# Kernel optimization log

Hardware: AMD Instinct MI355X
Metric: run time of the kernel (lower is better)

## Reference

```python
import jax, jax.numpy as jnp
import numpy as np

N = 4096
E = 262144
IN_C = 128
OUT_C = 128
EDGE_D = 16


def setup_inputs() -> dict:
    key = jax.random.key(0)
    k = jax.random.split(key, 8)
    x = jax.random.normal(k[0], (N, IN_C), dtype=jnp.float32)
    edge_index = jax.random.randint(k[1], (2, E), 0, N, dtype=jnp.int64)
    edge_attr = jax.random.normal(k[2], (N, N, EDGE_D), dtype=jnp.float32)
    # nn.Linear params: y = x @ W.T + b; store pre-transposed W for x @ W
    s1 = 1.0 / np.sqrt(IN_C + EDGE_D)
    s2 = 1.0 / np.sqrt(OUT_C)
    W1 = jax.random.uniform(k[3], (IN_C + EDGE_D, OUT_C), jnp.float32, -s1, s1)
    b1 = jax.random.uniform(k[4], (OUT_C,), jnp.float32, -s1, s1)
    W2 = jax.random.uniform(k[5], (OUT_C, OUT_C), jnp.float32, -s2, s2)
    b2 = jax.random.uniform(k[6], (OUT_C,), jnp.float32, -s2, s2)
    return {"x": x, "edge_index": edge_index, "edge_attr": edge_attr,
            "W1": W1, "b1": b1, "W2": W2, "b2": b2}


def reference(x, edge_index, edge_attr, W1, b1, W2, b2):
    row, col = edge_index[0], edge_index[1]
    x_row = x[row]                      # [E, IN_C] gather
    e = edge_attr[row, col]             # [E, EDGE_D] gather from dense NxN table
    h = jnp.concatenate([x_row, e], axis=-1)     # [E, IN_C+EDGE_D]
    h = jax.nn.relu(h @ W1 + b1)                  # [E, OUT_C]
    h = jax.nn.relu(h @ W2 + b2)                  # [E, OUT_C]
    # global_add_pool(out, col): scatter-add edges into node buckets by col
    return jax.ops.segment_sum(h, col, num_segments=x.shape[0])  # [N, OUT_C]
```

## Files before the change

kernel.cpp:

```cpp
#include <hip/hip_runtime.h>
#include <hip/hip_bf16.h>

#define NN 4096
#define IC 128
#define OC 128
#define ED 16
#define EPB 128
#define NT 512
#define NSLOT 8
#define NBLK 256

typedef __bf16 bf16x8 __attribute__((ext_vector_type(8)));
typedef float  f32x4  __attribute__((ext_vector_type(4)));

#define BAR() do { asm volatile("s_waitcnt lgkmcnt(0)" ::: "memory"); \
    __builtin_amdgcn_s_barrier(); \
    __builtin_amdgcn_sched_barrier(0); } while (0)

__device__ __forceinline__ unsigned short bf16u(float f) {
    unsigned int u = __float_as_uint(f);
    u = (u + 0x7FFFu + ((u >> 16) & 1u)) >> 16;
    return (unsigned short)u;
}
__device__ __forceinline__ float bf16tof(unsigned short h) {
    return __uint_as_float(((unsigned int)h) << 16);
}
__device__ __forceinline__ int swzk(int row) { return (row ^ (row >> 3)) & 7; }

__global__ __launch_bounds__(128) void k_xw1(
    const float* __restrict__ x, const float* __restrict__ W1,
    const float* __restrict__ b1, float* __restrict__ xw1b,
    float* __restrict__ out, int* __restrict__ hist)
{
    __shared__ float xs[8][IC];
    const int t = threadIdx.x;
    const int r0 = blockIdx.x * 8;
    #pragma unroll
    for (int r = 0; r < 8; ++r) xs[r][t] = x[(size_t)(r0 + r) * IC + t];

    const float4 z = make_float4(0.f, 0.f, 0.f, 0.f);
    float4* o4 = (float4*)out;
    o4[blockIdx.x * 256 + t]       = z;
    o4[blockIdx.x * 256 + 128 + t] = z;
    if (blockIdx.x == 0) {
        int4* h4 = (int4*)hist;
        #pragma unroll
        for (int j = 0; j < 8; ++j) h4[j * 128 + t] = make_int4(0, 0, 0, 0);
    }

    __syncthreads();
    float acc[8];
    const float bb = b1[t];
    #pragma unroll
    for (int r = 0; r < 8; ++r) acc[r] = bb;
    #pragma unroll 4
    for (int k = 0; k < IC; ++k) {
        const float w = W1[(size_t)k * OC + t];
        #pragma unroll
        for (int r = 0; r < 8; ++r) acc[r] = fmaf(xs[r][k], w, acc[r]);
    }
    #pragma unroll
    for (int r = 0; r < 8; ++r) xw1b[(size_t)(r0 + r) * OC + t] = acc[r];
}

__global__ void k_hist(const int* __restrict__ eidx, int* __restrict__ hist, int E) {
    const int i = blockIdx.x * blockDim.x + threadIdx.x;
    if (i < E) atomicAdd(&hist[eidx[E + i]], 1);
}

__global__ __launch_bounds__(256) void k_scan(
    const int* __restrict__ hist, int* __restrict__ cursor)
{
    __shared__ int tot[256];
    __shared__ int base[256];
    const int t = threadIdx.x;
    int loc[16];
    int s = 0;
    #pragma unroll
    for (int j = 0; j < 16; ++j) { loc[j] = s; s += hist[t * 16 + j]; }
    tot[t] = s;
    __syncthreads();
    if (t == 0) {
        int a = 0;
        for (int i = 0; i < 256; ++i) { base[i] = a; a += tot[i]; }
    }
    __syncthreads();
    const int b = base[t];
    #pragma unroll
    for (int j = 0; j < 16; ++j) cursor[t * 16 + j] = b + loc[j];
}

__global__ void k_scatter(const int* __restrict__ eidx, int* __restrict__ cursor,
                          int2* __restrict__ csr, int E) {
    const int i = blockIdx.x * blockDim.x + threadIdx.x;
    if (i < E) {
        const int row = eidx[i];
        const int col = eidx[E + i];
        const int pos = atomicAdd(&cursor[col], 1);
        csr[pos] = make_int2(row, col);
    }
}

__global__ __launch_bounds__(NT, 2) void k_edge6(
    const int2* __restrict__ csr, const float* __restrict__ eattr,
    const float* __restrict__ xw1b, const float* __restrict__ W1,
    const float* __restrict__ W2, const float* __restrict__ b2,
    float* __restrict__ out, int E)
{
    extern __shared__ char smem[];
    char*   const W2hi = smem;
    char*   const W2lo = smem + 32768;
    char*   const h1hi = smem + 65536;
    char*   const h1lo = smem + 98304;
    float4* const eaL  = (float4*)(smem + 131072);
    float4* const w1L  = (float4*)(smem + 139264);
    float*  const lacc = (float*)(smem + 147456);
    int*    const srowL = (int*)(smem + 151552);
    int*    const scolL = srowL + 256;

    const int t   = threadIdx.x;
    const int l   = t & 63;
    const int wid = t >> 6;
    const int cg  = t & 15, eg = t >> 4;
    const int c0  = cg << 3, e0 = eg << 2;
    const int sz  = (eg >> 1) & 3;
    const int em  = t >> 2, q = t & 3;
    const int esz = (em >> 3) & 3;

    w1L[t] = ((const float4*)(W1 + (size_t)IC * OC))[t];
    {
        const int n = t >> 2, kh = (t & 3) * 32;
        const int key = swzk(n) << 4;
        for (int j0 = 0; j0 < 32; j0 += 8) {
            union { unsigned short us[8]; uint4 qv; } Hh, Hl;
            #pragma unroll
            for (int j = 0; j < 8; ++j) {
                const float w = W2[(size_t)(kh + j0 + j) * OC + n];
                const unsigned short h = bf16u(w);
                Hh.us[j] = h;
                Hl.us[j] = bf16u(w - bf16tof(h));
            }
            const int a = n * 256 + (((kh + j0) * 2) ^ key);
            *(uint4*)(W2hi + a) = Hh.qv;
            *(uint4*)(W2lo + a) = Hl.qv;
        }
    }
    float b2r[8];
    #pragma unroll
    for (int nr = 0; nr < 8; ++nr) b2r[nr] = b2[nr * 16 + (l & 15)];

    const int nper = (E / EPB) / NBLK;
    const int ibb  = blockIdx.x * nper;

    if (t < EPB) {
        const int2 rc = csr[(size_t)ibb * EPB + t];
        srowL[t] = rc.x;
        scolL[t] = rc.y;
    }
    __syncthreads();

    float4 pA;
    {
        const int r = srowL[em], c = scolL[em];
        pA = ((const float4*)(eattr + ((size_t)r * NN + c) * ED))[q];
    }
    float4 xa[4], xb[4];
    #pragma unroll
    for (int ri = 0; ri < 4; ++ri) {
        const int row = srowL[e0 + ri];
        const float4* p = (const float4*)(xw1b + (size_t)row * OC + c0);
        xa[ri] = p[0]; xb[ri] = p[1];
    }
    int2 pidx;
    {
        const int ibn = (nper > 1) ? 1 : 0;
        pidx = (t < EPB) ? csr[(size_t)(ibb + ibn) * EPB + t] : make_int2(0, 0);
    }

    int cur = 0;
    for (int ii = 0; ii < nper; ++ii) {
        const int nxt = cur ^ 1;

        BAR();

        lacc[t] = 0.f; lacc[t + NT] = 0.f;
        if (t < EPB) { srowL[nxt * 128 + t] = pidx.x; scolL[nxt * 128 + t] = pidx.y; }
        eaL[(em * 4 + q) ^ esz] = pA;
        BAR();

        float4 ha[4], hb[4];
        #pragma unroll
        for (int ri = 0; ri < 4; ++ri) { ha[ri] = xa[ri]; hb[ri] = xb[ri]; }
        #pragma unroll
        for (int dc = 0; dc < 4; ++dc) {
            float4 ev[4];
            #pragma unroll
            for (int ri = 0; ri < 4; ++ri)
                ev[ri] = eaL[((e0 + ri) * 4 + dc) ^ sz];
            #pragma unroll
            for (int dd = 0; dd < 4; ++dd) {
                const int d = dc * 4 + dd;
                const float4 wA = w1L[d * 32 + cg * 2];
                const float4 wB = w1L[d * 32 + cg * 2 + 1];
                #pragma unroll
                for (int ri = 0; ri < 4; ++ri) {
                    const float evd = (dd == 0) ? ev[ri].x : (dd == 1) ? ev[ri].y
                                     : (dd == 2) ? ev[ri].z : ev[ri].w;
                    ha[ri].x = fmaf(evd, wA.x, ha[ri].x);
                    ha[ri].y = fmaf(evd, wA.y, ha[ri].y);
                    ha[ri].z = fmaf(evd, wA.z, ha[ri].z);
                    ha[ri].w = fmaf(evd, wA.w, ha[ri].w);
                    hb[ri].x = fmaf(evd, wB.x, hb[ri].x);
                    hb[ri].y = fmaf(evd, wB.y, hb[ri].y);
                    hb[ri].z = fmaf(evd, wB.z, hb[ri].z);
                    hb[ri].w = fmaf(evd, wB.w, hb[ri].w);
                }
            }
        }
        #pragma unroll
        for (int ri = 0; ri < 4; ++ri) {
            const int row = e0 + ri;
            float v[8] = { ha[ri].x, ha[ri].y, ha[ri].z, ha[ri].w,
                           hb[ri].x, hb[ri].y, hb[ri].z, hb[ri].w };
            union { unsigned short us[8]; uint4 qv; } Hh, Hl;
            #pragma unroll
            for (int j = 0; j < 8; ++j) {
                const float f = fmaxf(v[j], 0.f);
                const unsigned short h = bf16u(f);
                Hh.us[j] = h;
                Hl.us[j] = bf16u(f - bf16tof(h));
            }
            const int boff = (cg * 16) ^ (swzk(row) << 4);
            *(uint4*)(h1hi + row * 256 + boff) = Hh.qv;
            *(uint4*)(h1lo + row * 256 + boff) = Hl.qv;
        }

        {
            const int r = srowL[nxt * 128 + em], c = scolL[nxt * 128 + em];
            pA = ((const float4*)(eattr + ((size_t)r * NN + c) * ED))[q];
        }
        #pragma unroll
        for (int ri = 0; ri < 4; ++ri) {
            const int row = srowL[nxt * 128 + e0 + ri];
            const float4* p = (const float4*)(xw1b + (size_t)row * OC + c0);
            xa[ri] = p[0]; xb[ri] = p[1];
        }
        {
            const int iin = (ii + 2 < nper) ? (ii + 2) : (nper - 1);
            pidx = (t < EPB) ? csr[(size_t)(ibb + iin) * EPB + t] : make_int2(0, 0);
        }
        BAR();

        f32x4 acc[8];
        #pragma unroll
        for (int nr = 0; nr < 8; ++nr) acc[nr] = (f32x4){0.f, 0.f, 0.f, 0.f};
        const int arow = wid * 16 + (l & 15);
        const int akey = swzk(arow) << 4;
        #pragma unroll
        for (int kc = 0; kc < 4; ++kc) {
            const int kb = kc * 64 + ((l >> 4) << 4);
            const bf16x8 aH = *(const bf16x8*)(h1hi + arow * 256 + (kb ^ akey));
            const bf16x8 aL = *(const bf16x8*)(h1lo + arow * 256 + (kb ^ akey));
            #pragma unroll
            for (int nr = 0; nr < 8; ++nr) {
                const int brow = nr * 16 + (l & 15);
                const int ba = brow * 256 + (kb ^ (swzk(brow) << 4));
                const bf16x8 bH = *(const bf16x8*)(W2hi + ba);
                const bf16x8 bL = *(const bf16x8*)(W2lo + ba);
                acc[nr] = __builtin_amdgcn_mfma_f32_16x16x32_bf16(aH, bH, acc[nr], 0, 0, 0);
                acc[nr] = __builtin_amdgcn_mfma_f32_16x16x32_bf16(aL, bH, acc[nr], 0, 0, 0);
                acc[nr] = __builtin_amdgcn_mfma_f32_16x16x32_bf16(aH, bL, acc[nr], 0, 0, 0);
            }
        }

        const int colbase = scolL[cur * 128];
        {
            const int eb = wid * 16 + ((l >> 4) << 2);
            float s[8];
            int ccur = scolL[cur * 128 + eb];
            #pragma unroll
            for (int nr = 0; nr < 8; ++nr)
                s[nr] = fmaxf(acc[nr][0] + b2r[nr], 0.f);
            #pragma unroll
            for (int r = 1; r < 4; ++r) {
                const int c = scolL[cur * 128 + eb + r];
                if (c != ccur) {
                    const int slot = ccur - colbase;
                    if (slot < NSLOT) {
                        #pragma unroll
                        for (int nr = 0; nr < 8; ++nr)
                            if (s[nr] != 0.f)
                                atomicAdd(&lacc[slot * OC + nr * 16 + (l & 15)], s[nr]);
                    } else {
                        #pragma unroll
                        for (int nr = 0; nr < 8; ++nr)
                            if (s[nr] != 0.f)
                                atomicAdd(&out[(size_t)ccur * OC + nr * 16 + (l & 15)], s[nr]);
                    }
                    ccur = c;
                    #pragma unroll
                    for (int nr = 0; nr < 8; ++nr)
                        s[nr] = fmaxf(acc[nr][r] + b2r[nr], 0.f);
                } else {
                    #pragma unroll
                    for (int nr = 0; nr < 8; ++nr)
                        s[nr] += fmaxf(acc[nr][r] + b2r[nr], 0.f);
                }
            }
            {
                const int slot = ccur - colbase;
                if (slot < NSLOT) {
                    #pragma unroll
                    for (int nr = 0; nr < 8; ++nr)
                        if (s[nr] != 0.f)
                            atomicAdd(&lacc[slot * OC + nr * 16 + (l & 15)], s[nr]);
                } else {
                    #pragma unroll
                    for (int nr = 0; nr < 8; ++nr)
                        if (s[nr] != 0.f)
                            atomicAdd(&out[(size_t)ccur * OC + nr * 16 + (l & 15)], s[nr]);
                }
            }
        }
        BAR();

        int span = scolL[cur * 128 + 127] - colbase + 1;
        if (span > NSLOT) span = NSLOT;
        for (int idx = t; idx < span * OC; idx += NT) {
            const float v = lacc[idx];
            if (v != 0.f)
                atomicAdd(&out[(size_t)(colbase + (idx >> 7)) * OC + (idx & 127)], v);
        }
        cur = nxt;
    }
}

#define LDS_BYTES 153600

extern "C" void kernel_launch(void* const* d_in, const int* in_sizes, int n_in,
                              void* d_out, int out_size, void* d_ws, size_t ws_size,
                              hipStream_t stream) {
    const float* x    = (const float*)d_in[0];
    const int*   eidx = (const int*)d_in[1];
    const float* ea   = (const float*)d_in[2];
    const float* W1   = (const float*)d_in[3];
    const float* b1   = (const float*)d_in[4];
    const float* W2   = (const float*)d_in[5];
    const float* b2   = (const float*)d_in[6];
    float* out = (float*)d_out;

    const int E = in_sizes[1] / 2;

    char* ws = (char*)d_ws;
    float* xw1b   = (float*)ws;
    int*   hist   = (int*)(ws + 2097152);
    int*   cursor = (int*)(ws + 2097152 + 16384);
    int2*  csr    = (int2*)(ws + 2097152 + 32768);

    k_xw1<<<NN / 8, 128, 0, stream>>>(x, W1, b1, xw1b, out, hist);
    k_hist<<<(E + 255) / 256, 256, 0, stream>>>(eidx, hist, E);
    k_scan<<<1, 256, 0, stream>>>(hist, cursor);
    k_scatter<<<(E + 255) / 256, 256, 0, stream>>>(eidx, cursor, csr, E);

    hipFuncSetAttribute(reinterpret_cast<const void*>(k_edge6),
                        hipFuncAttributeMaxDynamicSharedMemorySize, LDS_BYTES);
    k_edge6<<<NBLK, NT, LDS_BYTES, stream>>>(csr, ea, xw1b, W1, W2, b2, out, E);
}
```

Baseline: 151.6 us.

## Keep W2 in registers and switch second GEMM to 32x32x16 MFMA tiles

```diff
diff --git a/kernel.cpp b/kernel.cpp
--- a/kernel.cpp
+++ b/kernel.cpp
@@ -11,7 +11,7 @@
 #define NBLK 256
 
 typedef __bf16 bf16x8 __attribute__((ext_vector_type(8)));
-typedef float  f32x4  __attribute__((ext_vector_type(4)));
+typedef float  f32x16 __attribute__((ext_vector_type(16)));
 
 #define BAR() do { asm volatile("s_waitcnt lgkmcnt(0)" ::: "memory"); \
     __builtin_amdgcn_s_barrier(); \
@@ -101,21 +101,19 @@
     }
 }
 
-__global__ __launch_bounds__(NT, 2) void k_edge6(
+__global__ __launch_bounds__(NT, 2) void k_edge7(
     const int2* __restrict__ csr, const float* __restrict__ eattr,
     const float* __restrict__ xw1b, const float* __restrict__ W1,
     const float* __restrict__ W2, const float* __restrict__ b2,
     float* __restrict__ out, int E)
 {
     extern __shared__ char smem[];
-    char*   const W2hi = smem;
-    char*   const W2lo = smem + 32768;
-    char*   const h1hi = smem + 65536;
-    char*   const h1lo = smem + 98304;
-    float4* const eaL  = (float4*)(smem + 131072);
-    float4* const w1L  = (float4*)(smem + 139264);
-    float*  const lacc = (float*)(smem + 147456);
-    int*    const srowL = (int*)(smem + 151552);
+    char*   const h1hi = smem;
+    char*   const h1lo = smem + 32768;
+    float4* const eaL  = (float4*)(smem + 65536);
+    float4* const w1L  = (float4*)(smem + 73728);
+    float*  const lacc = (float*)(smem + 81920);
+    int*    const srowL = (int*)(smem + 86016);
     int*    const scolL = srowL + 256;
 
     const int t   = threadIdx.x;
@@ -127,27 +125,30 @@
     const int em  = t >> 2, q = t & 3;
     const int esz = (em >> 3) & 3;
 
+    const int ntl = wid & 3;
+    const int mh  = wid >> 2;
+    const int lm  = l & 31;
+    const int hi  = l >> 5;
+    const int c2  = ntl * 32 + lm;
+
     w1L[t] = ((const float4*)(W1 + (size_t)IC * OC))[t];
-    {
-        const int n = t >> 2, kh = (t & 3) * 32;
-        const int key = swzk(n) << 4;
-        for (int j0 = 0; j0 < 32; j0 += 8) {
-            union { unsigned short us[8]; uint4 qv; } Hh, Hl;
-            #pragma unroll
-            for (int j = 0; j < 8; ++j) {
-                const float w = W2[(size_t)(kh + j0 + j) * OC + n];
-                const unsigned short h = bf16u(w);
-                Hh.us[j] = h;
-                Hl.us[j] = bf16u(w - bf16tof(h));
-            }
-            const int a = n * 256 + (((kh + j0) * 2) ^ key);
-            *(uint4*)(W2hi + a) = Hh.qv;
-            *(uint4*)(W2lo + a) = Hl.qv;
-        }
-    }
-    float b2r[8];
-    #pragma unroll
-    for (int nr = 0; nr < 8; ++nr) b2r[nr] = b2[nr * 16 + (l & 15)];
+
+    bf16x8 w2h[8], w2l[8];
+    #pragma unroll
+    for (int s = 0; s < 8; ++s) {
+        union { unsigned short us[8]; bf16x8 v; } Uh, Ul;
+        #pragma unroll
+        for (int j = 0; j < 8; ++j) {
+            const float w = W2[(size_t)(s * 16 + hi * 8 + j) * OC + c2];
+            const unsigned short h = bf16u(w);
+            Uh.us[j] = h;
+            Ul.us[j] = bf16u(w - bf16tof(h));
+        }
+        w2h[s] = Uh.v; w2l[s] = Ul.v;
+    }
+    const float b2s = b2[c2];
+
+    lacc[t] = 0.f; lacc[t + NT] = 0.f;
 
     const int nper = (E / EPB) / NBLK;
     const int ibb  = blockIdx.x * nper;
@@ -164,13 +165,6 @@
         const int r = srowL[em], c = scolL[em];
         pA = ((const float4*)(eattr + ((size_t)r * NN + c) * ED))[q];
     }
-    float4 xa[4], xb[4];
-    #pragma unroll
-    for (int ri = 0; ri < 4; ++ri) {
-        const int row = srowL[e0 + ri];
-        const float4* p = (const float4*)(xw1b + (size_t)row * OC + c0);
-        xa[ri] = p[0]; xb[ri] = p[1];
-    }
     int2 pidx;
     {
         const int ibn = (nper > 1) ? 1 : 0;
@@ -183,9 +177,15 @@
 
         BAR();
 
-        lacc[t] = 0.f; lacc[t + NT] = 0.f;
         if (t < EPB) { srowL[nxt * 128 + t] = pidx.x; scolL[nxt * 128 + t] = pidx.y; }
         eaL[(em * 4 + q) ^ esz] = pA;
+        float4 xa[4], xb[4];
+        #pragma unroll
+        for (int ri = 0; ri < 4; ++ri) {
+            const int row = srowL[cur * 128 + e0 + ri];
+            const float4* p = (const float4*)(xw1b + (size_t)row * OC + c0);
+            xa[ri] = p[0]; xb[ri] = p[1];
+        }
         BAR();
 
         float4 ha[4], hb[4];
@@ -234,91 +234,72 @@
             *(uint4*)(h1hi + row * 256 + boff) = Hh.qv;
             *(uint4*)(h1lo + row * 256 + boff) = Hl.qv;
         }
-
         {
             const int r = srowL[nxt * 128 + em], c = scolL[nxt * 128 + em];
             pA = ((const float4*)(eattr + ((size_t)r * NN + c) * ED))[q];
         }
-        #pragma unroll
-        for (int ri = 0; ri < 4; ++ri) {
-            const int row = srowL[nxt * 128 + e0 + ri];
-            const float4* p = (const float4*)(xw1b + (size_t)row * OC + c0);
-            xa[ri] = p[0]; xb[ri] = p[1];
-        }
         {
             const int iin = (ii + 2 < nper) ? (ii + 2) : (nper - 1);
             pidx = (t < EPB) ? csr[(size_t)(ibb + iin) * EPB + t] : make_int2(0, 0);
         }
         BAR();
 
-        f32x4 acc[8];
-        #pragma unroll
-        for (int nr = 0; nr < 8; ++nr) acc[nr] = (f32x4){0.f, 0.f, 0.f, 0.f};
-        const int arow = wid * 16 + (l & 15);
-        const int akey = swzk(arow) << 4;
-        #pragma unroll
-        for (int kc = 0; kc < 4; ++kc) {
-            const int kb = kc * 64 + ((l >> 4) << 4);
-            const bf16x8 aH = *(const bf16x8*)(h1hi + arow * 256 + (kb ^ akey));
-            const bf16x8 aL = *(const bf16x8*)(h1lo + arow * 256 + (kb ^ akey));
+        f32x16 acc0 = (f32x16)(0.0f);
+        f32x16 acc1 = (f32x16)(0.0f);
+        const int arow0 = (mh * 2 + 0) * 32 + lm;
+        const int arow1 = (mh * 2 + 1) * 32 + lm;
+        const int ak0 = swzk(arow0) << 4;
+        const int ak1 = swzk(arow1) << 4;
+        #pragma unroll
+        for (int s = 0; s < 8; ++s) {
+            const int kb = s * 32 + hi * 16;
+            const bf16x8 aH0 = *(const bf16x8*)(h1hi + arow0 * 256 + (kb ^ ak0));
+            const bf16x8 aL0 = *(const bf16x8*)(h1lo + arow0 * 256 + (kb ^ ak0));
+            const bf16x8 aH1 = *(const bf16x8*)(h1hi + arow1 * 256 + (kb ^ ak1));
+            const bf16x8 aL1 = *(const bf16x8*)(h1lo + arow1 * 256 + (kb ^ ak1));
+            acc0 = __builtin_amdgcn_mfma_f32_32x32x16_bf16(aH0, w2h[s], acc0, 0, 0, 0);
+            acc1 = __builtin_amdgcn_mfma_f32_32x32x16_bf16(aH1, w2h[s], acc1, 0, 0, 0);
+            acc0 = __builtin_amdgcn_mfma_f32_32x32x16_bf16(aL0, w2h[s], acc0, 0, 0, 0);
+            acc1 = __builtin_amdgcn_mfma_f32_32x32x16_bf16(aL1, w2h[s], acc1, 0, 0, 0);
+            acc0 = __builtin_amdgcn_mfma_f32_32x32x16_bf16(aH0, w2l[s], acc0, 0, 0, 0);
+            acc1 = __builtin_amdgcn_mfma_f32_32x32x16_bf16(aH1, w2l[s], acc1, 0, 0, 0);
+        }
+
+        const int colbase = scolL[cur * 128];
+        #pragma unroll
+        for (int p = 0; p < 2; ++p) {
+            const int mbase = (mh * 2 + p) * 32 + 4 * hi;
             #pragma unroll
-            for (int nr = 0; nr < 8; ++nr) {
-                const int brow = nr * 16 + (l & 15);
-                const int ba = brow * 256 + (kb ^ (swzk(brow) << 4));
-                const bf16x8 bH = *(const bf16x8*)(W2hi + ba);
-                const bf16x8 bL = *(const bf16x8*)(W2lo + ba);
-                acc[nr] = __builtin_amdgcn_mfma_f32_16x16x32_bf16(aH, bH, acc[nr], 0, 0, 0);
-                acc[nr] = __builtin_amdgcn_mfma_f32_16x16x32_bf16(aL, bH, acc[nr], 0, 0, 0);
-                acc[nr] = __builtin_amdgcn_mfma_f32_16x16x32_bf16(aH, bL, acc[nr], 0, 0, 0);
-            }
-        }
-
-        const int colbase = scolL[cur * 128];
-        {
-            const int eb = wid * 16 + ((l >> 4) << 2);
-            float s[8];
-            int ccur = scolL[cur * 128 + eb];
-            #pragma unroll
-            for (int nr = 0; nr < 8; ++nr)
-                s[nr] = fmaxf(acc[nr][0] + b2r[nr], 0.f);
-            #pragma unroll
-            for (int r = 1; r < 4; ++r) {
-                const int c = scolL[cur * 128 + eb + r];
-                if (c != ccur) {
-                    const int slot = ccur - colbase;
-                    if (slot < NSLOT) {
-                        #pragma unroll
-                        for (int nr = 0; nr < 8; ++nr)
-                            if (s[nr] != 0.f)
-                                atomicAdd(&lacc[slot * OC + nr * 16 + (l & 15)], s[nr]);
+            for (int g = 0; g < 4; ++g) {
+                const int eb = mbase + 8 * g;
+                float sv;
+                {
+                    const float a0 = (p == 0) ? acc0[4 * g] : acc1[4 * g];
+                    sv = fmaxf(a0 + b2s, 0.f);
+                }
+                int ccur = scolL[cur * 128 + eb];
+                #pragma unroll
+                for (int j = 1; j < 4; ++j) {
+                    const float aj = (p == 0) ? acc0[4 * g + j] : acc1[4 * g + j];
+                    const float v = fmaxf(aj + b2s, 0.f);
+                    const int c = scolL[cur * 128 + eb + j];
+                    if (c == ccur) {
+                        sv += v;
                     } else {
-                        #pragma unroll
-                        for (int nr = 0; nr < 8; ++nr)
-                            if (s[nr] != 0.f)
-                                atomicAdd(&out[(size_t)ccur * OC + nr * 16 + (l & 15)], s[nr]);
+                        const int slot = ccur - colbase;
+                        if (slot < NSLOT) {
+                            if (sv != 0.f) atomicAdd(&lacc[slot * OC + c2], sv);
+                        } else {
+                            if (sv != 0.f) atomicAdd(&out[(size_t)ccur * OC + c2], sv);
+                        }
+                        ccur = c; sv = v;
                     }
-                    ccur = c;
-                    #pragma unroll
-                    for (int nr = 0; nr < 8; ++nr)
-                        s[nr] = fmaxf(acc[nr][r] + b2r[nr], 0.f);
-                } else {
-                    #pragma unroll
-                    for (int nr = 0; nr < 8; ++nr)
-                        s[nr] += fmaxf(acc[nr][r] + b2r[nr], 0.f);
                 }
-            }
-            {
                 const int slot = ccur - colbase;
                 if (slot < NSLOT) {
-                    #pragma unroll
-                    for (int nr = 0; nr < 8; ++nr)
-                        if (s[nr] != 0.f)
-                            atomicAdd(&lacc[slot * OC + nr * 16 + (l & 15)], s[nr]);
+                    if (sv != 0.f) atomicAdd(&lacc[slot * OC + c2], sv);
                 } else {
-                    #pragma unroll
-                    for (int nr = 0; nr < 8; ++nr)
-                        if (s[nr] != 0.f)
-                            atomicAdd(&out[(size_t)ccur * OC + nr * 16 + (l & 15)], s[nr]);
+                    if (sv != 0.f) atomicAdd(&out[(size_t)ccur * OC + c2], sv);
                 }
             }
         }
@@ -328,6 +309,7 @@
         if (span > NSLOT) span = NSLOT;
         for (int idx = t; idx < span * OC; idx += NT) {
             const float v = lacc[idx];
+            lacc[idx] = 0.f;
             if (v != 0.f)
                 atomicAdd(&out[(size_t)(colbase + (idx >> 7)) * OC + (idx & 127)], v);
         }
@@ -335,7 +317,7 @@
     }
 }
 
-#define LDS_BYTES 153600
+#define LDS_BYTES 88064
 
 extern "C" void kernel_launch(void* const* d_in, const int* in_sizes, int n_in,
                               void* d_out, int out_size, void* d_ws, size_t ws_size,
@@ -362,7 +344,7 @@
     k_scan<<<1, 256, 0, stream>>>(hist, cursor);
     k_scatter<<<(E + 255) / 256, 256, 0, stream>>>(eidx, cursor, csr, E);
 
-    hipFuncSetAttribute(reinterpret_cast<const void*>(k_edge6),
+    hipFuncSetAttribute(reinterpret_cast<const void*>(k_edge7),
                         hipFuncAttributeMaxDynamicSharedMemorySize, LDS_BYTES);
-    k_edge6<<<NBLK, NT, LDS_BYTES, stream>>>(csr, ea, xw1b, W1, W2, b2, out, E);
-}
+    k_edge7<<<NBLK, NT, LDS_BYTES, stream>>>(csr, ea, xw1b, W1, W2, b2, out, E);
+}
```

New measurement: 150.4 us. Within noise of the previous version (-0.8%).
